# Optimization experiments

Hardware: AMD Instinct MI355X
Metric: run time of the kernel (lower is better)

Reference implementation:

```python
import jax, jax.numpy as jnp
import numpy as np

N0, C1, C2 = 100000, 10000, 1000
E0 = 1_600_000
IN = 128
H = 128
OUT = 128


def _pool_edges(ei, ew, cluster, C):
    # PyG pool_edge: remap via cluster, drop self loops, coalesce (sum weights)
    m = cluster[ei]
    mask = m[0] != m[1]
    m = m[:, mask]
    w = ew[mask]
    keys = m[0] * C + m[1]
    uk, inv = np.unique(keys, return_inverse=True)
    w2 = np.bincount(inv, weights=w).astype(np.float32)
    return np.stack([uk // C, uk % C]).astype(np.int64), w2


def _with_self_loops(ei, ew, N):
    # gcn_norm(add_remaining_self_loops, fill_value=1); base edges have no loops
    row = np.concatenate([ei[0], np.arange(N)]).astype(np.int64)
    col = np.concatenate([ei[1], np.arange(N)]).astype(np.int64)
    w = np.concatenate([ew, np.ones(N, np.float32)])
    return row, col, w


def setup_inputs() -> dict:
    rng = np.random.default_rng(0)
    ei = rng.integers(0, N0, size=(2, E0))
    ei = ei[:, ei[0] != ei[1]]
    ew = np.ones(ei.shape[1], np.float32)
    # guaranteed-surjective cluster assignments (stand-in for Louvain output)
    c1 = rng.permutation(np.arange(N0) % C1).astype(np.int64)
    c2 = rng.permutation(np.arange(C1) % C2).astype(np.int64)
    ei1, ew1 = _pool_edges(ei, ew, c1, C1)
    ei2, ew2 = _pool_edges(ei1, ew1, c2, C2)
    r0, co0, w0 = _with_self_loops(ei, ew, N0)
    r1, co1, w1 = _with_self_loops(ei1, ew1, C1)
    r2, co2, w2 = _with_self_loops(ei2, ew2, C2)

    key = jax.random.key(0)
    ks = jax.random.split(key, 16)
    def lin(k, fi, fo):
        return jax.random.normal(k, (fi, fo), jnp.float32) / np.sqrt(fi)
    inp = {
        'x': jax.random.normal(ks[0], (N0, IN), jnp.float32),
        'W_pre': lin(ks[1], IN, H), 'b_pre': jnp.zeros((H,), jnp.float32),
        'W_u0': lin(ks[2], H, H), 'b_u0': jnp.zeros((H,), jnp.float32),
        'W_u1': lin(ks[3], H, H), 'b_u1': jnp.zeros((H,), jnp.float32),
        'W_u2': lin(ks[4], H, H), 'b_u2': jnp.zeros((H,), jnp.float32),
        'W_d0': lin(ks[5], H, OUT), 'b_d0': jnp.zeros((OUT,), jnp.float32),
        'W_d1': lin(ks[6], H, H), 'b_d1': jnp.zeros((H,), jnp.float32),
        'row0': jnp.asarray(r0), 'col0': jnp.asarray(co0), 'ew0': jnp.asarray(w0),
        'row1': jnp.asarray(r1), 'col1': jnp.asarray(co1), 'ew1': jnp.asarray(w1),
        'row2': jnp.asarray(r2), 'col2': jnp.asarray(co2), 'ew2': jnp.asarray(w2),
        'cluster1': jnp.asarray(c1), 'cluster2': jnp.asarray(c2),
    }
    return inp


def _gcn(x, W, b, row, col, ew, N):
    # PyG GCNConv: sym-normalized aggregation at target (col)
    deg = jax.ops.segment_sum(ew, col, num_segments=N)
    dinv = jnp.where(deg > 0, jax.lax.rsqrt(deg), 0.0)
    norm = dinv[row] * ew * dinv[col]
    h = x @ W                                   # [N, F_out]
    out = jax.ops.segment_sum(h[row] * norm[:, None], col, num_segments=N)
    return out + b


def _seg_mean(x, cluster, C):
    s = jax.ops.segment_sum(x, cluster, num_segments=C)
    cnt = jax.ops.segment_sum(jnp.ones((x.shape[0], 1), x.dtype), cluster,
                              num_segments=C)
    return s / jnp.maximum(cnt, 1.0)


def reference(x, W_pre, b_pre, W_u0, b_u0, W_u1, b_u1, W_u2, b_u2,
              W_d0, b_d0, W_d1, b_d1,
              row0, col0, ew0, row1, col1, ew1, row2, col2, ew2,
              cluster1, cluster2):
    # --- up (coarsening) path ---
    h = x @ W_pre + b_pre                                   # preembed
    x0 = jax.nn.relu(_gcn(h, W_u0, b_u0, row0, col0, ew0, N0))
    x1 = _seg_mean(x0, cluster1, C1)                        # avg_pool level 1
    x1 = jax.nn.relu(_gcn(x1, W_u1, b_u1, row1, col1, ew1, C1))
    x2 = _seg_mean(x1, cluster2, C2)                        # avg_pool level 2
    x2 = jax.nn.relu(_gcn(x2, W_u2, b_u2, row2, col2, ew2, C2))
    # --- down (unpooling) path; down convs use all-ones edge weights ---
    y = x1 + x2[cluster2]
    y = jax.nn.relu(_gcn(y, W_d1, b_d1, row1, col1, jnp.ones_like(ew1), C1))
    y = x0 + y[cluster1]
    y = _gcn(y, W_d0, b_d0, row0, col0, jnp.ones_like(ew0), N0)
    return y
```

## Files before the change

### kernel.cpp

```cpp
#include <hip/hip_runtime.h>

#define HH 128
static constexpr int kN0 = 100000;
static constexpr int kC1 = 10000;
static constexpr int kC2 = 1000;

static constexpr int B0 = kN0;
static constexpr int B1 = B0 + kC1;
static constexpr int B2 = B1 + kC2;
static constexpr int B3 = B2 + kC1;
static constexpr int NTOT = B3 + kC2;

static constexpr int NB0 = (kN0 + 127) / 128;
static constexpr int NB1 = (kC1 + 7) / 8;
static constexpr int NB2 = kC2;
static constexpr int NBP1 = (kC1 + 127) / 128;
static constexpr int NBP2 = (kC2 + 15) / 16;
static constexpr int Q0 = NB0;
static constexpr int Q1 = Q0 + NB1;
static constexpr int Q2 = Q1 + NB2;
static constexpr int Q3 = Q2 + NBP1;
static constexpr int NBK = Q3 + NBP2;

static constexpr int P3_BLOCKS = 128;

__device__ __forceinline__ int bucket_of(int bin) {
  if (bin < B0) return bin >> 7;
  if (bin < B1) return Q0 + ((bin - B0) >> 3);
  if (bin < B2) return Q1 + (bin - B1);
  if (bin < B3) return Q2 + ((bin - B2) >> 7);
  return Q3 + ((bin - B3) >> 4);
}

__device__ __forceinline__ unsigned int f2_to_bf2(float a, float b) {
  unsigned int ua = __float_as_uint(a);
  unsigned int ub = __float_as_uint(b);
  ua = (ua + 0x7fffu + ((ua >> 16) & 1u)) >> 16;
  ub = (ub + 0x7fffu + ((ub >> 16) & 1u)) & 0xffff0000u;
  return ua | ub;
}
__device__ __forceinline__ unsigned short f2bf(float f) {
  unsigned int u = __float_as_uint(f);
  u = (u + 0x7fffu + ((u >> 16) & 1u)) >> 16;
  return (unsigned short)u;
}
__device__ __forceinline__ float bf2f(unsigned short s) {
  return __uint_as_float(((unsigned int)s) << 16);
}

using bf16x8 = __attribute__((ext_vector_type(8))) short;
using f32x4 = __attribute__((ext_vector_type(4))) float;

__global__ __launch_bounds__(256) void p1_kernel(const int* __restrict__ col0,
                                                 const int* __restrict__ col1,
                                                 const int* __restrict__ col2,
                                                 const int* __restrict__ cl1,
                                                 const int* __restrict__ cl2,
                                                 int E0, int E1, int E2,
                                                 int* __restrict__ bucketCnt) {
  __shared__ int h[NBK];
  for (int i = threadIdx.x; i < NBK; i += 256) h[i] = 0;
  __syncthreads();
  int T0 = E0, T1 = T0 + E1, T2 = T1 + E2, T3 = T2 + kN0, T4 = T3 + kC1;
  for (int g = blockIdx.x * 256 + threadIdx.x; g < T4; g += gridDim.x * 256) {
    int bin;
    if (g < T0)      bin = col0[g];
    else if (g < T1) bin = B0 + col1[g - T0];
    else if (g < T2) bin = B1 + col2[g - T1];
    else if (g < T3) bin = B2 + cl1[g - T2];
    else             bin = B3 + cl2[g - T3];
    atomicAdd(&h[bucket_of(bin)], 1);
  }
  __syncthreads();
  for (int i = threadIdx.x; i < NBK; i += 256) {
    int c = h[i];
    if (c) atomicAdd(&bucketCnt[i], c);
  }
}

__global__ __launch_bounds__(1024) void p2_kernel(const int* __restrict__ bucketCnt,
                                                  int* __restrict__ bucketStart,
                                                  int* __restrict__ cursor,
                                                  int* __restrict__ startsg, int T) {
  int t = threadIdx.x;
  int v[4]; int s = 0;
#pragma unroll
  for (int j = 0; j < 4; j++) {
    int i = t * 4 + j;
    v[j] = (i < NBK) ? bucketCnt[i] : 0;
    s += v[j];
  }
  int lane = t & 63, w = t >> 6;
  int incl = s;
  for (int o = 1; o < 64; o <<= 1) { int u = __shfl_up(incl, o); if (lane >= o) incl += u; }
  __shared__ int wt[16];
  if (lane == 63) wt[w] = incl;
  __syncthreads();
  if (t == 0) { int run = 0; for (int i = 0; i < 16; i++) { int c = wt[i]; wt[i] = run; run += c; } }
  __syncthreads();
  int ex = wt[w] + incl - s;
#pragma unroll
  for (int j = 0; j < 4; j++) {
    int i = t * 4 + j;
    if (i < NBK) { bucketStart[i] = ex; cursor[i] = ex; }
    ex += v[j];
  }
  if (t == 0) { bucketStart[NBK] = T; startsg[NTOT] = T; }
}

__global__ __launch_bounds__(256) void p3_kernel(const int* __restrict__ col0,
                                                 const int* __restrict__ col1,
                                                 const int* __restrict__ col2,
                                                 const int* __restrict__ cl1,
                                                 const int* __restrict__ cl2,
                                                 const int* __restrict__ row0,
                                                 const int* __restrict__ row1,
                                                 const int* __restrict__ row2,
                                                 const float* __restrict__ ew1,
                                                 const float* __restrict__ ew2,
                                                 int E0, int E1, int E2,
                                                 int* __restrict__ cursor,
                                                 int4* __restrict__ part) {
  __shared__ int h[NBK];
  for (int i = threadIdx.x; i < NBK; i += 256) h[i] = 0;
  __syncthreads();
  int T0 = E0, T1 = T0 + E1, T2 = T1 + E2, T3 = T2 + kN0, T4 = T3 + kC1;
  int chunk = ((T4 + P3_BLOCKS - 1) / P3_BLOCKS + 255) & ~255;
  int start = blockIdx.x * chunk;
  int end = start + chunk; if (end > T4) end = T4;
  for (int g = start + (int)threadIdx.x; g < end; g += 256) {
    int bin;
    if (g < T0)      bin = col0[g];
    else if (g < T1) bin = B0 + col1[g - T0];
    else if (g < T2) bin = B1 + col2[g - T1];
    else if (g < T3) bin = B2 + cl1[g - T2];
    else             bin = B3 + cl2[g - T3];
    atomicAdd(&h[bucket_of(bin)], 1);
  }
  __syncthreads();
  for (int i = threadIdx.x; i < NBK; i += 256) {
    int c = h[i];
    h[i] = c ? atomicAdd(&cursor[i], c) : 0;
  }
  __syncthreads();
  for (int g = start + (int)threadIdx.x; g < end; g += 256) {
    int bin, src; float w = 0.f;
    if (g < T0)      { bin = col0[g]; src = row0[g]; }
    else if (g < T1) { int e = g - T0; bin = B0 + col1[e]; src = row1[e]; w = ew1[e]; }
    else if (g < T2) { int e = g - T1; bin = B1 + col2[e]; src = row2[e]; w = ew2[e]; }
    else if (g < T3) { int e = g - T2; bin = B2 + cl1[e]; src = e; }
    else             { int e = g - T3; bin = B3 + cl2[e]; src = e; }
    int slot = atomicAdd(&h[bucket_of(bin)], 1);
    part[slot] = make_int4(bin, src, __float_as_int(w), 0);
  }
}

__global__ __launch_bounds__(256) void p4_kernel(const int* __restrict__ bucketStart,
                                                 const int4* __restrict__ part,
                                                 int* __restrict__ startsg,
                                                 int* __restrict__ rowS,
                                                 float* __restrict__ ewSm) {
  int b = blockIdx.x;
  int binLo, width;
  if (b < Q0)      { binLo = b << 7;                 width = 128; if (binLo + width > B0) width = B0 - binLo; }
  else if (b < Q1) { binLo = B0 + ((b - Q0) << 3);   width = 8; }
  else if (b < Q2) { binLo = B1 + (b - Q1);          width = 1; }
  else if (b < Q3) { binLo = B2 + ((b - Q2) << 7);   width = 128; if (binLo + width > B3) width = B3 - binLo; }
  else             { binLo = B3 + ((b - Q3) << 4);   width = 16; if (binLo + width > NTOT) width = NTOT - binLo; }
  int base = bucketStart[b], nend = bucketStart[b + 1];
  int t = threadIdx.x;

  if (width == 1) {
    if (t == 0) startsg[binLo] = base;
    bool isEw = (binLo >= B0 && binLo < B2);
    for (int i = base + t; i < nend; i += 256) {
      int4 it = part[i];
      rowS[i] = it.y;
      if (isEw) ewSm[i] = __int_as_float(it.z);
    }
    return;
  }

  __shared__ int h[128];
  __shared__ int cur[128];
  if (t < 128) h[t] = 0;
  __syncthreads();
  for (int i = base + t; i < nend; i += 256) atomicAdd(&h[part[i].x - binLo], 1);
  __syncthreads();
  if (t == 0) {
    int run = 0;
    for (int j = 0; j < width; j++) {
      cur[j] = run;
      startsg[binLo + j] = base + run;
      run += h[j];
    }
  }
  __syncthreads();
  for (int i = base + t; i < nend; i += 256) {
    int4 it = part[i];
    int k = it.x;
    int r = atomicAdd(&cur[k - binLo], 1);
    int dst = base + r;
    rowS[dst] = it.y;
    if (k >= B0 && k < B2) ewSm[dst] = __int_as_float(it.z);
  }
}

__global__ void dinv_kernel(const int* __restrict__ startsg, const float* __restrict__ ewSm,
                            float* __restrict__ d0, float* __restrict__ d1w,
                            float* __restrict__ d1o, float* __restrict__ d2) {
  int t = blockIdx.x * 256 + threadIdx.x;
  if (t < kN0) {
    int c = startsg[t + 1] - startsg[t];
    d0[t] = c > 0 ? rsqrtf((float)c) : 0.f;
  }
  int wid = t >> 6, lane = t & 63;
  if (wid < kC1) {
    int s = startsg[B0 + wid], e = startsg[B0 + wid + 1];
    float a = 0.f;
    for (int k = s + lane; k < e; k += 64) a += ewSm[k];
    for (int o = 32; o > 0; o >>= 1) a += __shfl_down(a, o);
    if (lane == 0) {
      d1w[wid] = a > 0.f ? rsqrtf(a) : 0.f;
      int c = e - s;
      d1o[wid] = c > 0 ? rsqrtf((float)c) : 0.f;
    }
  } else if (wid < kC1 + kC2) {
    int w2 = wid - kC1;
    int s = startsg[B1 + w2], e = startsg[B1 + w2 + 1];
    float a = 0.f;
    for (int k = s + lane; k < e; k += 64) a += ewSm[k];
    for (int o = 32; o > 0; o >>= 1) a += __shfl_down(a, o);
    if (lane == 0) d2[w2] = a > 0.f ? rsqrtf(a) : 0.f;
  }
}

__global__ void wprep_kernel(const int* __restrict__ rowS, const float* __restrict__ ewSm,
                             const float* __restrict__ d1w, const float* __restrict__ d2,
                             int E0, int E1, int E2,
                             float* __restrict__ wAll) {
  int e = blockIdx.x * 256 + threadIdx.x + E0;
  int tot = E0 + E1 + E2;
  if (e >= tot) return;
  int r = rowS[e];
  if (e < E0 + E1) {
    wAll[e] = d1w[r] * ewSm[e];
  } else {
    wAll[e] = d2[r] * ewSm[e];
  }
}

__global__ __launch_bounds__(256) void matmul_kernel(const float* __restrict__ X,
                                                     const float* __restrict__ Xadd,
                                                     const int* __restrict__ cl,
                                                     const float* __restrict__ W,
                                                     const float* __restrict__ bias,
                                                     const float* __restrict__ rowScale,
                                                     float* __restrict__ Y,
                                                     unsigned int* __restrict__ Ybf, int N) {
  __shared__ float Ws[64 * 128];
  __shared__ float Xs[32 * 128];
  int t = threadIdx.x;
  int rbase = blockIdx.x * 32;
  const float4* X4 = (const float4*)X;
  float4* Xs4 = (float4*)Xs;
#pragma unroll
  for (int i = 0; i < 4; i++) {
    int idx = t + 256 * i;
    int fr = idx >> 5, fc = idx & 31;
    int row = rbase + fr; if (row >= N) row = N - 1;
    float4 v = X4[(size_t)row * 32 + fc];
    if (Xadd) {
      int c = cl[row];
      float4 u = ((const float4*)Xadd)[(size_t)c * 32 + fc];
      v.x += u.x; v.y += u.y; v.z += u.z; v.w += u.w;
    }
    Xs4[idx] = v;
  }
  float acc[4][4];
#pragma unroll
  for (int r = 0; r < 4; r++)
#pragma unroll
    for (int cc = 0; cc < 4; cc++) acc[r][cc] = 0.f;
  int c0 = (t & 31) * 4;
  int rl = (t >> 5) * 4;
  const float4* W4 = (const float4*)W;
  float4* Ws4 = (float4*)Ws;
  for (int half = 0; half < 2; half++) {
    __syncthreads();
#pragma unroll
    for (int i = 0; i < 8; i++) {
      int idx = t + 256 * i;
      Ws4[idx] = W4[half * 2048 + idx];
    }
    __syncthreads();
#pragma unroll 4
    for (int k = 0; k < 64; k++) {
      float4 w4 = *(const float4*)(Ws + k * 128 + c0);
      float xv[4];
#pragma unroll
      for (int r = 0; r < 4; r++) xv[r] = Xs[(rl + r) * 128 + half * 64 + k];
#pragma unroll
      for (int r = 0; r < 4; r++) {
        acc[r][0] = fmaf(xv[r], w4.x, acc[r][0]);
        acc[r][1] = fmaf(xv[r], w4.y, acc[r][1]);
        acc[r][2] = fmaf(xv[r], w4.z, acc[r][2]);
        acc[r][3] = fmaf(xv[r], w4.w, acc[r][3]);
      }
    }
  }
  float4 b4 = make_float4(0.f, 0.f, 0.f, 0.f);
  if (bias) b4 = *(const float4*)(bias + c0);
#pragma unroll
  for (int r = 0; r < 4; r++) {
    int row = rbase + rl + r;
    if (row < N) {
      float sc = rowScale ? rowScale[row] : 1.f;
      float4 o;
      o.x = (acc[r][0] + b4.x) * sc; o.y = (acc[r][1] + b4.y) * sc;
      o.z = (acc[r][2] + b4.z) * sc; o.w = (acc[r][3] + b4.w) * sc;
      if (Ybf) {
        unsigned int pk0 = f2_to_bf2(o.x, o.y);
        unsigned int pk1 = f2_to_bf2(o.z, o.w);
        *(uint2*)(Ybf + (size_t)row * 64 + (c0 >> 1)) = make_uint2(pk0, pk1);
      } else {
        *(float4*)(Y + (size_t)row * 128 + c0) = o;
      }
    }
  }
}

__global__ __launch_bounds__(256, 2) void mfma_gemm_kernel(
    const float* __restrict__ X, const float* __restrict__ Xadd,
    const int* __restrict__ cl, const float* __restrict__ W,
    const float* __restrict__ bias, const float* __restrict__ rowScale,
    unsigned int* __restrict__ Ybf, int N) {
  __shared__ unsigned int Bt[128 * 64];
  int t = threadIdx.x;
  {
    int n = t & 127, kh = t >> 7;
#pragma unroll
    for (int k = kh * 64; k < kh * 64 + 64; k += 2) {
      float a = W[(size_t)k * 128 + n];
      float b = W[(size_t)(k + 1) * 128 + n];
      unsigned int pk = (unsigned int)f2bf(a) | ((unsigned int)f2bf(b) << 16);
      unsigned int byteoff = ((unsigned int)(n * 256 + k * 2)) ^ (((unsigned int)n & 7u) << 4);
      *(unsigned int*)((char*)Bt + byteoff) = pk;
    }
  }
  __syncthreads();
  int wv = t >> 6, lane = t & 63;
  int g = lane >> 4, mrow = lane & 15;
  int rbase = blockIdx.x * 128 + wv * 32;
  bf16x8 ahi[2][4], alo[2][4];
#pragma unroll
  for (int mt = 0; mt < 2; mt++) {
    int row = rbase + mt * 16 + mrow;
    int rc = row < N ? row : N - 1;
    const float4* Xr = (const float4*)(X + (size_t)rc * 128);
    const float4* Ar = Xadd ? (const float4*)(Xadd + (size_t)cl[rc] * 128) : nullptr;
#pragma unroll
    for (int ks = 0; ks < 4; ks++) {
      int c4 = ks * 8 + g * 2;
      float4 v0 = Xr[c4], v1 = Xr[c4 + 1];
      if (Ar) {
        float4 u0 = Ar[c4], u1 = Ar[c4 + 1];
        v0.x += u0.x; v0.y += u0.y; v0.z += u0.z; v0.w += u0.w;
        v1.x += u1.x; v1.y += u1.y; v1.z += u1.z; v1.w += u1.w;
      }
      float vv[8] = {v0.x, v0.y, v0.z, v0.w, v1.x, v1.y, v1.z, v1.w};
      bf16x8 h, l;
#pragma unroll
      for (int j = 0; j < 8; j++) {
        unsigned short hb = f2bf(vv[j]);
        h[j] = (short)hb;
        l[j] = (short)f2bf(vv[j] - bf2f(hb));
      }
      ahi[mt][ks] = h; alo[mt][ks] = l;
    }
  }
  f32x4 acc[2][8];
#pragma unroll
  for (int mt = 0; mt < 2; mt++)
#pragma unroll
    for (int nt = 0; nt < 8; nt++) acc[mt][nt] = (f32x4){0.f, 0.f, 0.f, 0.f};
#pragma unroll
  for (int ks = 0; ks < 4; ks++) {
#pragma unroll
    for (int nt = 0; nt < 8; nt++) {
      int n = nt * 16 + mrow;
      unsigned int byteoff =
          ((unsigned int)(n * 256 + ks * 64 + g * 16)) ^ (((unsigned int)n & 7u) << 4);
      bf16x8 b = *(const bf16x8*)((const char*)Bt + byteoff);
      acc[0][nt] = __builtin_amdgcn_mfma_f32_16x16x32_bf16(ahi[0][ks], b, acc[0][nt], 0, 0, 0);
      acc[1][nt] = __builtin_amdgcn_mfma_f32_16x16x32_bf16(ahi[1][ks], b, acc[1][nt], 0, 0, 0);
      acc[0][nt] = __builtin_amdgcn_mfma_f32_16x16x32_bf16(alo[0][ks], b, acc[0][nt], 0, 0, 0);
      acc[1][nt] = __builtin_amdgcn_mfma_f32_16x16x32_bf16(alo[1][ks], b, acc[1][nt], 0, 0, 0);
    }
  }
#pragma unroll
  for (int mt = 0; mt < 2; mt++) {
#pragma unroll
    for (int r = 0; r < 4; r++) {
      int row = rbase + mt * 16 + g * 4 + r;
      if (row < N) {
        float sc = rowScale ? rowScale[row] : 1.f;
#pragma unroll
        for (int nt = 0; nt < 4; nt++) {
          int c = nt * 16 + mrow;
          float lo = (acc[mt][nt][r] + (bias ? bias[c] : 0.f)) * sc;
          float hi = (acc[mt][nt + 4][r] + (bias ? bias[c + 64] : 0.f)) * sc;
          Ybf[(size_t)row * 64 + c] = (unsigned int)f2bf(lo) | ((unsigned int)f2bf(hi) << 16);
        }
      }
    }
  }
}

__global__ __launch_bounds__(256) void agg_kernel(const unsigned int* __restrict__ Hf,
                                                  float* __restrict__ out,
                                                  const int* __restrict__ starts,
                                                  const int* __restrict__ rowS,
                                                  const float* __restrict__ dinv,
                                                  const float* __restrict__ bias,
                                                  int C, int relu) {
  int wid = (blockIdx.x * blockDim.x + threadIdx.x) >> 6;
  int lane = threadIdx.x & 63;
  if (wid >= C) return;
  int h = lane >> 5, hl = lane & 31;
  const uint2* Hf2 = (const uint2*)Hf;
  int s = starts[wid], e = starts[wid + 1];
  float dc = dinv[wid];
  float a0 = 0.f, a1 = 0.f, b0 = 0.f, b1 = 0.f;
  for (int base = s; base < e; base += 64) {
    int n = e - base; if (n > 64) n = 64;
    int r = rowS[base + (lane < n ? lane : 0)];
    for (int j = 0; j < n; j += 16) {
#pragma unroll
      for (int u = 0; u < 8; u++) {
        int eidx = j + u * 2 + h;
        bool v = eidx < n;
        int rr = __shfl(r, v ? eidx : 0);
        uint2 pv = Hf2[(size_t)rr * 32 + hl];
        if (!v) { pv.x = 0u; pv.y = 0u; }
        a0 += __uint_as_float(pv.x << 16);
        b0 += __uint_as_float(pv.x & 0xffff0000u);
        a1 += __uint_as_float(pv.y << 16);
        b1 += __uint_as_float(pv.y & 0xffff0000u);
      }
    }
  }
  a0 += __shfl_xor(a0, 32); a1 += __shfl_xor(a1, 32);
  b0 += __shfl_xor(b0, 32); b1 += __shfl_xor(b1, 32);
  int c0 = h * 64 + hl * 2;
  float o0 = (h ? b0 : a0) * dc + bias[c0];
  float o1 = (h ? b1 : a1) * dc + bias[c0 + 1];
  if (relu) { o0 = fmaxf(o0, 0.f); o1 = fmaxf(o1, 0.f); }
  *(float2*)(out + (size_t)wid * 128 + c0) = make_float2(o0, o1);
}

__global__ __launch_bounds__(256) void aggb_kernel(const unsigned int* __restrict__ Hf,
                                                   float* __restrict__ out,
                                                   const int* __restrict__ starts,
                                                   const int* __restrict__ rowS,
                                                   const float* __restrict__ wS,
                                                   const float* __restrict__ dinv,
                                                   const float* __restrict__ bias,
                                                   int C, int relu) {
  int node = blockIdx.x;
  if (node >= C) return;
  int wv = threadIdx.x >> 6, lane = threadIdx.x & 63;
  int h = lane >> 5, hl = lane & 31;
  const uint2* Hf2 = (const uint2*)Hf;
  int s = starts[node], e = starts[node + 1];
  float a0 = 0.f, a1 = 0.f, a2 = 0.f, a3 = 0.f;
  for (int base = s + wv * 64; base < e; base += 256) {
    int n = e - base; if (n > 64) n = 64;
    int moff = base + (lane < n ? lane : 0);
    int r = rowS[moff];
    float w = wS[moff];
    for (int j = 0; j < n; j += 16) {
#pragma unroll
      for (int u = 0; u < 8; u++) {
        int eidx = j + u * 2 + h;
        bool v = eidx < n;
        int rr = __shfl(r, v ? eidx : 0);
        float ww = __shfl(w, v ? eidx : 0);
        if (!v) ww = 0.f;
        uint2 pv = Hf2[(size_t)rr * 32 + hl];
        a0 = fmaf(ww, __uint_as_float(pv.x << 16), a0);
        a1 = fmaf(ww, __uint_as_float(pv.x & 0xffff0000u), a1);
        a2 = fmaf(ww, __uint_as_float(pv.y << 16), a2);
        a3 = fmaf(ww, __uint_as_float(pv.y & 0xffff0000u), a3);
      }
    }
  }
  a0 += __shfl_xor(a0, 32); a1 += __shfl_xor(a1, 32);
  a2 += __shfl_xor(a2, 32); a3 += __shfl_xor(a3, 32);
  __shared__ float4 sh[4][32];
  if (h == 0) sh[wv][hl] = make_float4(a0, a1, a2, a3);
  __syncthreads();
  if (threadIdx.x < 32) {
    float4 v0 = sh[0][threadIdx.x], v1 = sh[1][threadIdx.x];
    float4 v2 = sh[2][threadIdx.x], v3 = sh[3][threadIdx.x];
    float dc = dinv[node];
    int c0 = threadIdx.x * 4;
    float4 bb = *(const float4*)(bias + c0);
    float4 o;
    o.x = (v0.x + v1.x + v2.x + v3.x) * dc + bb.x;
    o.y = (v0.y + v1.y + v2.y + v3.y) * dc + bb.y;
    o.z = (v0.z + v1.z + v2.z + v3.z) * dc + bb.z;
    o.w = (v0.w + v1.w + v2.w + v3.w) * dc + bb.w;
    if (relu) {
      o.x = fmaxf(o.x, 0.f); o.y = fmaxf(o.y, 0.f);
      o.z = fmaxf(o.z, 0.f); o.w = fmaxf(o.w, 0.f);
    }
    *(float4*)(out + (size_t)node * 128 + c0) = o;
  }
}

__global__ __launch_bounds__(256) void aggb1_kernel(const unsigned int* __restrict__ Hf,
                                                    float* __restrict__ out,
                                                    const int* __restrict__ starts,
                                                    const int* __restrict__ rowS,
                                                    const float* __restrict__ dinv,
                                                    const float* __restrict__ bias,
                                                    int C, int relu) {
  int node = blockIdx.x;
  if (node >= C) return;
  int wv = threadIdx.x >> 6, lane = threadIdx.x & 63;
  int h = lane >> 5, hl = lane & 31;
  const uint2* Hf2 = (const uint2*)Hf;
  int s = starts[node], e = starts[node + 1];
  float a0 = 0.f, a1 = 0.f, a2 = 0.f, a3 = 0.f;
  for (int base = s + wv * 64; base < e; base += 256) {
    int n = e - base; if (n > 64) n = 64;
    int r = rowS[base + (lane < n ? lane : 0)];
    for (int j = 0; j < n; j += 16) {
#pragma unroll
      for (int u = 0; u < 8; u++) {
        int eidx = j + u * 2 + h;
        bool v = eidx < n;
        int rr = __shfl(r, v ? eidx : 0);
        uint2 pv = Hf2[(size_t)rr * 32 + hl];
        if (!v) { pv.x = 0u; pv.y = 0u; }
        a0 += __uint_as_float(pv.x << 16);
        a1 += __uint_as_float(pv.x & 0xffff0000u);
        a2 += __uint_as_float(pv.y << 16);
        a3 += __uint_as_float(pv.y & 0xffff0000u);
      }
    }
  }
  a0 += __shfl_xor(a0, 32); a1 += __shfl_xor(a1, 32);
  a2 += __shfl_xor(a2, 32); a3 += __shfl_xor(a3, 32);
  __shared__ float4 sh[4][32];
  if (h == 0) sh[wv][hl] = make_float4(a0, a1, a2, a3);
  __syncthreads();
  if (threadIdx.x < 32) {
    float4 v0 = sh[0][threadIdx.x], v1 = sh[1][threadIdx.x];
    float4 v2 = sh[2][threadIdx.x], v3 = sh[3][threadIdx.x];
    float dc = dinv[node];
    int c0 = threadIdx.x * 4;
    float4 bb = *(const float4*)(bias + c0);
    float4 o;
    o.x = (v0.x + v1.x + v2.x + v3.x) * dc + bb.x;
    o.y = (v0.y + v1.y + v2.y + v3.y) * dc + bb.y;
    o.z = (v0.z + v1.z + v2.z + v3.z) * dc + bb.z;
    o.w = (v0.w + v1.w + v2.w + v3.w) * dc + bb.w;
    if (relu) {
      o.x = fmaxf(o.x, 0.f); o.y = fmaxf(o.y, 0.f);
      o.z = fmaxf(o.z, 0.f); o.w = fmaxf(o.w, 0.f);
    }
    *(float4*)(out + (size_t)node * 128 + c0) = o;
  }
}

__global__ __launch_bounds__(256) void pool_kernel(const float* __restrict__ src,
                                                   float* __restrict__ out,
                                                   const int* __restrict__ starts,
                                                   const int* __restrict__ rowS, int C) {
  int wid = (blockIdx.x * blockDim.x + threadIdx.x) >> 6;
  int lane = threadIdx.x & 63;
  if (wid >= C) return;
  int s = starts[wid], e = starts[wid + 1];
  float ax0 = 0.f, ay0 = 0.f, ax1 = 0.f, ay1 = 0.f;
  int m = s;
  for (; m + 7 < e; m += 8) {
    int idx[8];
#pragma unroll
    for (int u = 0; u < 8; u++) idx[u] = rowS[m + u];
#pragma unroll
    for (int u = 0; u < 8; u++) {
      float2 v = *(const float2*)(src + (size_t)idx[u] * 128 + lane * 2);
      if (u & 1) { ax1 += v.x; ay1 += v.y; } else { ax0 += v.x; ay0 += v.y; }
    }
  }
  for (; m < e; m++) {
    int id = rowS[m];
    const float2 v = *(const float2*)(src + (size_t)id * 128 + lane * 2);
    ax0 += v.x; ay0 += v.y;
  }
  float inv = (e > s) ? 1.f / (float)(e - s) : 0.f;
  *(float2*)(out + (size_t)wid * 128 + lane * 2) =
      make_float2((ax0 + ax1) * inv, (ay0 + ay1) * inv);
}


extern "C" void kernel_launch(void* const* d_in, const int* in_sizes, int n_in,
                              void* d_out, int out_size, void* d_ws, size_t ws_size,
                              hipStream_t stream) {
  const float* x     = (const float*)d_in[0];
  const float* W_pre = (const float*)d_in[1];
  const float* b_pre = (const float*)d_in[2];
  const float* W_u0  = (const float*)d_in[3];
  const float* b_u0  = (const float*)d_in[4];
  const float* W_u1  = (const float*)d_in[5];
  const float* b_u1  = (const float*)d_in[6];
  const float* W_u2  = (const float*)d_in[7];
  const float* b_u2  = (const float*)d_in[8];
  const float* W_d0  = (const float*)d_in[9];
  const float* b_d0  = (const float*)d_in[10];
  const float* W_d1  = (const float*)d_in[11];
  const float* b_d1  = (const float*)d_in[12];
  const int* row0 = (const int*)d_in[13];
  const int* col0 = (const int*)d_in[14];
  const int* row1 = (const int*)d_in[16];
  const int* col1 = (const int*)d_in[17];
  const float* ew1 = (const float*)d_in[18];
  const int* row2 = (const int*)d_in[19];
  const int* col2 = (const int*)d_in[20];
  const float* ew2 = (const float*)d_in[21];
  const int* cluster1 = (const int*)d_in[22];
  const int* cluster2 = (const int*)d_in[23];
  int E0 = in_sizes[13], E1 = in_sizes[16], E2 = in_sizes[19];
  float* out = (float*)d_out;
  int Ttot = E0 + E1 + E2 + kN0 + kC1;
  int Etot = E0 + E1 + E2;

  char* basep = (char*)d_ws;
  size_t off = 0;
  auto alloc = [&](size_t bytes) -> char* {
    char* p = basep + off;
    off = (off + bytes + 255) & ~(size_t)255;
    return p;
  };
  int* bucketCnt = (int*)alloc((size_t)NBK * 4);
  size_t zero_bytes = off;
  int* bucketStart = (int*)alloc((size_t)(NBK + 1) * 4);
  int* cursor      = (int*)alloc((size_t)NBK * 4);
  int* startsg     = (int*)alloc((size_t)(NTOT + 1) * 4);
  int* rowS  = (int*)alloc((size_t)Ttot * 4);
  float* ewS = (float*)alloc((size_t)(E1 + E2) * 4);
  float* ewSm = ewS - E0;
  float* dinv0  = (float*)alloc((size_t)kN0 * 4);
  float* dinv1w = (float*)alloc((size_t)kC1 * 4);
  float* dinv1o = (float*)alloc((size_t)kC1 * 4);
  float* dinv2  = (float*)alloc((size_t)kC2 * 4);
  size_t watermark = off;
  int4* part = (int4*)alloc((size_t)Ttot * 16);
  off = watermark;
  float* wAll = (float*)alloc((size_t)Etot * 4);
  float* Wf   = (float*)alloc((size_t)128 * 128 * 4);
  float* bfv  = (float*)alloc((size_t)128 * 4);
  float* A    = (float*)alloc((size_t)kN0 * HH * 4);
  float* s1a  = (float*)alloc((size_t)kC1 * HH * 4);
  float* s1b  = (float*)alloc((size_t)kC1 * HH * 4);
  float* s2a  = (float*)alloc((size_t)kC2 * HH * 4);
  unsigned int* s1bb = (unsigned int*)alloc((size_t)kC1 * 64 * 4);
  unsigned int* s2bb = (unsigned int*)alloc((size_t)kC2 * 64 * 4);
  unsigned int* s1cb = (unsigned int*)alloc((size_t)kC1 * 64 * 4);
  unsigned int* tb   = (unsigned int*)alloc((size_t)kN0 * 64 * 4);
  unsigned int* t0   = (unsigned int*)d_out;

  hipMemsetAsync(d_ws, 0, zero_bytes, stream);

  auto cdiv = [](int a, int b) { return (a + b - 1) / b; };

  p1_kernel<<<256, 256, 0, stream>>>(col0, col1, col2, cluster1, cluster2, E0, E1, E2, bucketCnt);
  p2_kernel<<<1, 1024, 0, stream>>>(bucketCnt, bucketStart, cursor, startsg, Ttot);
  p3_kernel<<<P3_BLOCKS, 256, 0, stream>>>(col0, col1, col2, cluster1, cluster2,
                                           row0, row1, row2, ew1, ew2, E0, E1, E2,
                                           cursor, part);
  p4_kernel<<<NBK, 256, 0, stream>>>(bucketStart, part, startsg, rowS, ewSm);
  dinv_kernel<<<cdiv((kC1 + kC2) * 64, 256), 256, 0, stream>>>(startsg, ewSm, dinv0, dinv1w,
                                                               dinv1o, dinv2);
  wprep_kernel<<<cdiv(E1 + E2, 256), 256, 0, stream>>>(rowS, ewSm, dinv1w, dinv2,
                                                       E0, E1, E2, wAll);

  matmul_kernel<<<cdiv(128, 32), 256, 0, stream>>>(W_pre, nullptr, nullptr, W_u0, nullptr,
                                                   nullptr, Wf, nullptr, 128);
  matmul_kernel<<<1, 256, 0, stream>>>(b_pre, nullptr, nullptr, W_u0, nullptr,
                                       nullptr, bfv, nullptr, 1);
  mfma_gemm_kernel<<<cdiv(kN0, 128), 256, 0, stream>>>(x, nullptr, nullptr, Wf, bfv, dinv0,
                                                       t0, kN0);
  agg_kernel<<<cdiv(kN0, 4), 256, 0, stream>>>(t0, A, startsg, rowS, dinv0, b_u0, kN0, 1);
  pool_kernel<<<cdiv(kC1, 4), 256, 0, stream>>>(A, s1a, startsg + B2, rowS, kC1);
  matmul_kernel<<<cdiv(kC1, 32), 256, 0, stream>>>(s1a, nullptr, nullptr, W_u1, nullptr,
                                                   nullptr, nullptr, s1bb, kC1);
  aggb_kernel<<<kC1, 256, 0, stream>>>(s1bb, s1a, startsg + B0, rowS, wAll, dinv1w, b_u1, kC1, 1);
  pool_kernel<<<cdiv(kC2, 4), 256, 0, stream>>>(s1a, s2a, startsg + B3, rowS, kC2);
  matmul_kernel<<<cdiv(kC2, 32), 256, 0, stream>>>(s2a, nullptr, nullptr, W_u2, nullptr,
                                                   nullptr, nullptr, s2bb, kC2);
  aggb_kernel<<<kC2, 256, 0, stream>>>(s2bb, s2a, startsg + B1, rowS, wAll, dinv2, b_u2, kC2, 1);
  matmul_kernel<<<cdiv(kC1, 32), 256, 0, stream>>>(s1a, s2a, cluster2, W_d1, nullptr,
                                                   dinv1o, nullptr, s1cb, kC1);
  aggb1_kernel<<<kC1, 256, 0, stream>>>(s1cb, s1b, startsg + B0, rowS, dinv1o, b_d1, kC1, 1);
  mfma_gemm_kernel<<<cdiv(kN0, 128), 256, 0, stream>>>(A, s1b, cluster1, W_d0, nullptr, dinv0,
                                                       tb, kN0);
  agg_kernel<<<cdiv(kN0, 4), 256, 0, stream>>>(tb, out, startsg, rowS, dinv0, b_d0, kN0, 0);
}
```

Before: 787.8 us.

## Replace two-level bucket CSR build with direct atomic counting sort

Replaces the bucketed two-pass CSR construction (shared-memory bucket histograms, a staging int4 partition buffer, and a per-bucket local sort) with a plain per-node global atomic degree histogram, a three-kernel prefix scan, and a direct atomic scatter into rowS and edge weights. This removes the 16-byte-per-edge staging buffer and the second sort pass. In exchange, every edge does a global atomic on its destination counter, and the order of sources within each row becomes nondeterministic, so floating-point sums may vary slightly between runs.

```diff
diff --git a/kernel.cpp b/kernel.cpp
--- a/kernel.cpp
+++ b/kernel.cpp
@@ -11,26 +11,8 @@
 static constexpr int B3 = B2 + kC1;
 static constexpr int NTOT = B3 + kC2;
 
-static constexpr int NB0 = (kN0 + 127) / 128;
-static constexpr int NB1 = (kC1 + 7) / 8;
-static constexpr int NB2 = kC2;
-static constexpr int NBP1 = (kC1 + 127) / 128;
-static constexpr int NBP2 = (kC2 + 15) / 16;
-static constexpr int Q0 = NB0;
-static constexpr int Q1 = Q0 + NB1;
-static constexpr int Q2 = Q1 + NB2;
-static constexpr int Q3 = Q2 + NBP1;
-static constexpr int NBK = Q3 + NBP2;
-
-static constexpr int P3_BLOCKS = 128;
-
-__device__ __forceinline__ int bucket_of(int bin) {
-  if (bin < B0) return bin >> 7;
-  if (bin < B1) return Q0 + ((bin - B0) >> 3);
-  if (bin < B2) return Q1 + (bin - B1);
-  if (bin < B3) return Q2 + ((bin - B2) >> 7);
-  return Q3 + ((bin - B3) >> 4);
-}
+static constexpr int SCAN_CHUNK = 2048;
+static constexpr int NSCAN = (NTOT + SCAN_CHUNK - 1) / SCAN_CHUNK;
 
 __device__ __forceinline__ unsigned int f2_to_bf2(float a, float b) {
   unsigned int ua = __float_as_uint(a);
@@ -51,16 +33,13 @@
 using bf16x8 = __attribute__((ext_vector_type(8))) short;
 using f32x4 = __attribute__((ext_vector_type(4))) float;
 
-__global__ __launch_bounds__(256) void p1_kernel(const int* __restrict__ col0,
-                                                 const int* __restrict__ col1,
-                                                 const int* __restrict__ col2,
-                                                 const int* __restrict__ cl1,
-                                                 const int* __restrict__ cl2,
-                                                 int E0, int E1, int E2,
-                                                 int* __restrict__ bucketCnt) {
-  __shared__ int h[NBK];
-  for (int i = threadIdx.x; i < NBK; i += 256) h[i] = 0;
-  __syncthreads();
+__global__ __launch_bounds__(256) void hist_kernel(const int* __restrict__ col0,
+                                                   const int* __restrict__ col1,
+                                                   const int* __restrict__ col2,
+                                                   const int* __restrict__ cl1,
+                                                   const int* __restrict__ cl2,
+                                                   int E0, int E1, int E2,
+                                                   int* __restrict__ deg) {
   int T0 = E0, T1 = T0 + E1, T2 = T1 + E2, T3 = T2 + kN0, T4 = T3 + kC1;
   for (int g = blockIdx.x * 256 + threadIdx.x; g < T4; g += gridDim.x * 256) {
     int bin;
@@ -69,140 +48,90 @@
     else if (g < T2) bin = B1 + col2[g - T1];
     else if (g < T3) bin = B2 + cl1[g - T2];
     else             bin = B3 + cl2[g - T3];
-    atomicAdd(&h[bucket_of(bin)], 1);
-  }
+    atomicAdd(&deg[bin], 1);
+  }
+}
+
+__global__ __launch_bounds__(256) void scan1_kernel(const int* __restrict__ deg,
+                                                    int* __restrict__ bsum) {
+  int b = blockIdx.x, t = threadIdx.x;
+  int base = b * SCAN_CHUNK;
+  int s = 0;
+  for (int j = t; j < SCAN_CHUNK; j += 256) {
+    int i = base + j;
+    if (i < NTOT) s += deg[i];
+  }
+  int lane = t & 63, w = t >> 6;
+  for (int o = 32; o > 0; o >>= 1) s += __shfl_down(s, o);
+  __shared__ int ws[4];
+  if (lane == 0) ws[w] = s;
   __syncthreads();
-  for (int i = threadIdx.x; i < NBK; i += 256) {
-    int c = h[i];
-    if (c) atomicAdd(&bucketCnt[i], c);
-  }
-}
-
-__global__ __launch_bounds__(1024) void p2_kernel(const int* __restrict__ bucketCnt,
-                                                  int* __restrict__ bucketStart,
-                                                  int* __restrict__ cursor,
-                                                  int* __restrict__ startsg, int T) {
-  int t = threadIdx.x;
-  int v[4]; int s = 0;
-#pragma unroll
-  for (int j = 0; j < 4; j++) {
-    int i = t * 4 + j;
-    v[j] = (i < NBK) ? bucketCnt[i] : 0;
+  if (t == 0) bsum[b] = ws[0] + ws[1] + ws[2] + ws[3];
+}
+
+__global__ void scan2_kernel(int* __restrict__ bsum) {
+  if (threadIdx.x == 0) {
+    int run = 0;
+    for (int i = 0; i < NSCAN; i++) { int c = bsum[i]; bsum[i] = run; run += c; }
+  }
+}
+
+__global__ __launch_bounds__(256) void scan3_kernel(const int* __restrict__ deg,
+                                                    const int* __restrict__ bsum,
+                                                    int* __restrict__ startsg,
+                                                    int* __restrict__ cursor, int T) {
+  int b = blockIdx.x, t = threadIdx.x;
+  int base = b * SCAN_CHUNK + t * 8;
+  int v[8]; int s = 0;
+#pragma unroll
+  for (int j = 0; j < 8; j++) {
+    int i = base + j;
+    v[j] = (i < NTOT) ? deg[i] : 0;
     s += v[j];
   }
   int lane = t & 63, w = t >> 6;
   int incl = s;
   for (int o = 1; o < 64; o <<= 1) { int u = __shfl_up(incl, o); if (lane >= o) incl += u; }
-  __shared__ int wt[16];
+  __shared__ int wt[4];
   if (lane == 63) wt[w] = incl;
   __syncthreads();
-  if (t == 0) { int run = 0; for (int i = 0; i < 16; i++) { int c = wt[i]; wt[i] = run; run += c; } }
+  if (t == 0) { int run = 0; for (int i = 0; i < 4; i++) { int c = wt[i]; wt[i] = run; run += c; } }
   __syncthreads();
-  int ex = wt[w] + incl - s;
-#pragma unroll
-  for (int j = 0; j < 4; j++) {
-    int i = t * 4 + j;
-    if (i < NBK) { bucketStart[i] = ex; cursor[i] = ex; }
+  int ex = bsum[b] + wt[w] + incl - s;
+#pragma unroll
+  for (int j = 0; j < 8; j++) {
+    int i = base + j;
+    if (i < NTOT) { startsg[i] = ex; cursor[i] = ex; }
     ex += v[j];
   }
-  if (t == 0) { bucketStart[NBK] = T; startsg[NTOT] = T; }
-}
-
-__global__ __launch_bounds__(256) void p3_kernel(const int* __restrict__ col0,
-                                                 const int* __restrict__ col1,
-                                                 const int* __restrict__ col2,
-                                                 const int* __restrict__ cl1,
-                                                 const int* __restrict__ cl2,
-                                                 const int* __restrict__ row0,
-                                                 const int* __restrict__ row1,
-                                                 const int* __restrict__ row2,
-                                                 const float* __restrict__ ew1,
-                                                 const float* __restrict__ ew2,
-                                                 int E0, int E1, int E2,
-                                                 int* __restrict__ cursor,
-                                                 int4* __restrict__ part) {
-  __shared__ int h[NBK];
-  for (int i = threadIdx.x; i < NBK; i += 256) h[i] = 0;
-  __syncthreads();
+  if (b == 0 && t == 0) startsg[NTOT] = T;
+}
+
+__global__ __launch_bounds__(256) void scat_kernel(const int* __restrict__ col0,
+                                                   const int* __restrict__ col1,
+                                                   const int* __restrict__ col2,
+                                                   const int* __restrict__ cl1,
+                                                   const int* __restrict__ cl2,
+                                                   const int* __restrict__ row0,
+                                                   const int* __restrict__ row1,
+                                                   const int* __restrict__ row2,
+                                                   const float* __restrict__ ew1,
+                                                   const float* __restrict__ ew2,
+                                                   int E0, int E1, int E2,
+                                                   int* __restrict__ cursor,
+                                                   int* __restrict__ rowS,
+                                                   float* __restrict__ ewSm) {
   int T0 = E0, T1 = T0 + E1, T2 = T1 + E2, T3 = T2 + kN0, T4 = T3 + kC1;
-  int chunk = ((T4 + P3_BLOCKS - 1) / P3_BLOCKS + 255) & ~255;
-  int start = blockIdx.x * chunk;
-  int end = start + chunk; if (end > T4) end = T4;
-  for (int g = start + (int)threadIdx.x; g < end; g += 256) {
-    int bin;
-    if (g < T0)      bin = col0[g];
-    else if (g < T1) bin = B0 + col1[g - T0];
-    else if (g < T2) bin = B1 + col2[g - T1];
-    else if (g < T3) bin = B2 + cl1[g - T2];
-    else             bin = B3 + cl2[g - T3];
-    atomicAdd(&h[bucket_of(bin)], 1);
-  }
-  __syncthreads();
-  for (int i = threadIdx.x; i < NBK; i += 256) {
-    int c = h[i];
-    h[i] = c ? atomicAdd(&cursor[i], c) : 0;
-  }
-  __syncthreads();
-  for (int g = start + (int)threadIdx.x; g < end; g += 256) {
-    int bin, src; float w = 0.f;
+  for (int g = blockIdx.x * 256 + threadIdx.x; g < T4; g += gridDim.x * 256) {
+    int bin, src; float w = 0.f; bool hasW = false;
     if (g < T0)      { bin = col0[g]; src = row0[g]; }
-    else if (g < T1) { int e = g - T0; bin = B0 + col1[e]; src = row1[e]; w = ew1[e]; }
-    else if (g < T2) { int e = g - T1; bin = B1 + col2[e]; src = row2[e]; w = ew2[e]; }
+    else if (g < T1) { int e = g - T0; bin = B0 + col1[e]; src = row1[e]; w = ew1[e]; hasW = true; }
+    else if (g < T2) { int e = g - T1; bin = B1 + col2[e]; src = row2[e]; w = ew2[e]; hasW = true; }
     else if (g < T3) { int e = g - T2; bin = B2 + cl1[e]; src = e; }
     else             { int e = g - T3; bin = B3 + cl2[e]; src = e; }
-    int slot = atomicAdd(&h[bucket_of(bin)], 1);
-    part[slot] = make_int4(bin, src, __float_as_int(w), 0);
-  }
-}
-
-__global__ __launch_bounds__(256) void p4_kernel(const int* __restrict__ bucketStart,
-                                                 const int4* __restrict__ part,
-                                                 int* __restrict__ startsg,
-                                                 int* __restrict__ rowS,
-                                                 float* __restrict__ ewSm) {
-  int b = blockIdx.x;
-  int binLo, width;
-  if (b < Q0)      { binLo = b << 7;                 width = 128; if (binLo + width > B0) width = B0 - binLo; }
-  else if (b < Q1) { binLo = B0 + ((b - Q0) << 3);   width = 8; }
-  else if (b < Q2) { binLo = B1 + (b - Q1);          width = 1; }
-  else if (b < Q3) { binLo = B2 + ((b - Q2) << 7);   width = 128; if (binLo + width > B3) width = B3 - binLo; }
-  else             { binLo = B3 + ((b - Q3) << 4);   width = 16; if (binLo + width > NTOT) width = NTOT - binLo; }
-  int base = bucketStart[b], nend = bucketStart[b + 1];
-  int t = threadIdx.x;
-
-  if (width == 1) {
-    if (t == 0) startsg[binLo] = base;
-    bool isEw = (binLo >= B0 && binLo < B2);
-    for (int i = base + t; i < nend; i += 256) {
-      int4 it = part[i];
-      rowS[i] = it.y;
-      if (isEw) ewSm[i] = __int_as_float(it.z);
-    }
-    return;
-  }
-
-  __shared__ int h[128];
-  __shared__ int cur[128];
-  if (t < 128) h[t] = 0;
-  __syncthreads();
-  for (int i = base + t; i < nend; i += 256) atomicAdd(&h[part[i].x - binLo], 1);
-  __syncthreads();
-  if (t == 0) {
-    int run = 0;
-    for (int j = 0; j < width; j++) {
-      cur[j] = run;
-      startsg[binLo + j] = base + run;
-      run += h[j];
-    }
-  }
-  __syncthreads();
-  for (int i = base + t; i < nend; i += 256) {
-    int4 it = part[i];
-    int k = it.x;
-    int r = atomicAdd(&cur[k - binLo], 1);
-    int dst = base + r;
-    rowS[dst] = it.y;
-    if (k >= B0 && k < B2) ewSm[dst] = __int_as_float(it.z);
+    int slot = atomicAdd(&cursor[bin], 1);
+    rowS[slot] = src;
+    if (hasW) ewSm[slot] = w;
   }
 }
 
@@ -644,11 +573,11 @@
     off = (off + bytes + 255) & ~(size_t)255;
     return p;
   };
-  int* bucketCnt = (int*)alloc((size_t)NBK * 4);
+  int* deg = (int*)alloc((size_t)NTOT * 4);
   size_t zero_bytes = off;
-  int* bucketStart = (int*)alloc((size_t)(NBK + 1) * 4);
-  int* cursor      = (int*)alloc((size_t)NBK * 4);
-  int* startsg     = (int*)alloc((size_t)(NTOT + 1) * 4);
+  int* bsum    = (int*)alloc((size_t)64 * 4);
+  int* startsg = (int*)alloc((size_t)(NTOT + 1) * 4);
+  int* cursor  = (int*)alloc((size_t)NTOT * 4);
   int* rowS  = (int*)alloc((size_t)Ttot * 4);
   float* ewS = (float*)alloc((size_t)(E1 + E2) * 4);
   float* ewSm = ewS - E0;
@@ -656,9 +585,6 @@
   float* dinv1w = (float*)alloc((size_t)kC1 * 4);
   float* dinv1o = (float*)alloc((size_t)kC1 * 4);
   float* dinv2  = (float*)alloc((size_t)kC2 * 4);
-  size_t watermark = off;
-  int4* part = (int4*)alloc((size_t)Ttot * 16);
-  off = watermark;
   float* wAll = (float*)alloc((size_t)Etot * 4);
   float* Wf   = (float*)alloc((size_t)128 * 128 * 4);
   float* bfv  = (float*)alloc((size_t)128 * 4);
@@ -676,12 +602,13 @@
 
   auto cdiv = [](int a, int b) { return (a + b - 1) / b; };
 
-  p1_kernel<<<256, 256, 0, stream>>>(col0, col1, col2, cluster1, cluster2, E0, E1, E2, bucketCnt);
-  p2_kernel<<<1, 1024, 0, stream>>>(bucketCnt, bucketStart, cursor, startsg, Ttot);
-  p3_kernel<<<P3_BLOCKS, 256, 0, stream>>>(col0, col1, col2, cluster1, cluster2,
-                                           row0, row1, row2, ew1, ew2, E0, E1, E2,
-                                           cursor, part);
-  p4_kernel<<<NBK, 256, 0, stream>>>(bucketStart, part, startsg, rowS, ewSm);
+  hist_kernel<<<1024, 256, 0, stream>>>(col0, col1, col2, cluster1, cluster2, E0, E1, E2, deg);
+  scan1_kernel<<<NSCAN, 256, 0, stream>>>(deg, bsum);
+  scan2_kernel<<<1, 64, 0, stream>>>(bsum);
+  scan3_kernel<<<NSCAN, 256, 0, stream>>>(deg, bsum, startsg, cursor, Ttot);
+  scat_kernel<<<1024, 256, 0, stream>>>(col0, col1, col2, cluster1, cluster2,
+                                        row0, row1, row2, ew1, ew2, E0, E1, E2,
+                                        cursor, rowS, ewSm);
   dinv_kernel<<<cdiv((kC1 + kC2) * 64, 256), 256, 0, stream>>>(startsg, ewSm, dinv0, dinv1w,
                                                                dinv1o, dinv2);
   wprep_kernel<<<cdiv(E1 + E2, 256), 256, 0, stream>>>(rowS, ewSm, dinv1w, dinv2,
```

Result: slower. 920.7 us (+16.9%).
